# Kernel tuning notes

Hardware: AMD Instinct MI355X
Metric: run time of the kernel (lower is better)

The kernel has to match this reference:

```python
import jax, jax.numpy as jnp
import numpy as np

ALPHA = 0.2  # LeakyReLU negative slope (module init arg)


def setup_inputs() -> dict:
    key = jax.random.key(0)
    ks = jax.random.split(key, 5)
    b, w, K, E = 8, 256, 256, 512  # batch, window_size, n_features, embed (=2*window)
    x = jax.random.normal(ks[0], (b, w, K), dtype=jnp.float32)
    W = jax.random.normal(ks[1], (E, 2 * w), dtype=jnp.float32) * 0.05
    b_lin = jax.random.normal(ks[2], (E,), dtype=jnp.float32) * 0.05
    a = jax.random.normal(ks[3], (E,), dtype=jnp.float32) * 0.05
    bias = jax.random.normal(ks[4], (K, K), dtype=jnp.float32) * 0.05
    return {"x": x, "W": W, "b_lin": b_lin, "a": a, "bias": bias}


def reference(x, W, b_lin, a, bias):
    # x: (b, window, K) -> v: (b, K, window)
    v = jnp.transpose(x, (0, 2, 1))
    w = v.shape[2]
    # lin(concat(v_i, v_j)) == v_i @ Wl^T + v_j @ Wr^T + b_lin  (split weight)
    Wl, Wr = W[:, :w], W[:, w:]
    left = jnp.einsum('bkw,ew->bke', v, Wl)    # (b, K, E)
    right = jnp.einsum('bkw,ew->bke', v, Wr)   # (b, K, E)
    pre = left[:, :, None, :] + right[:, None, :, :] + b_lin  # (b, K, K, E)
    act = jax.nn.leaky_relu(pre, negative_slope=ALPHA)
    e = jnp.einsum('bije,e->bij', act, a) + bias               # (b, K, K)
    attn = jax.nn.softmax(e, axis=2)  # dropout p=0 in eval -> identity
    h = jax.nn.sigmoid(jnp.einsum('bij,bjw->biw', attn, v))    # (b, K, window)
    return jnp.transpose(h, (0, 2, 1))                          # (b, window, K)
```

## Files before the change

kernel.cpp:

```cpp
#include <hip/hip_runtime.h>
#include <math.h>

typedef float f32x4 __attribute__((ext_vector_type(4)));
typedef __bf16 bf16x8 __attribute__((ext_vector_type(8)));
typedef unsigned short u16x8 __attribute__((ext_vector_type(8)));

__device__ __forceinline__ unsigned short f2bf(float f) {
    union { float f; unsigned int u; } v; v.f = f;
    unsigned int u = v.u;
    return (unsigned short)((u + 0x7fffu + ((u >> 16) & 1u)) >> 16);
}
__device__ __forceinline__ float bf_lo(unsigned int d) {
    union { unsigned int u; float f; } v; v.u = d << 16; return v.f;
}
__device__ __forceinline__ float bf_hi(unsigned int d) {
    union { unsigned int u; float f; } v; v.u = d & 0xffff0000u; return v.f;
}
__device__ __forceinline__ unsigned int u4get(const uint4& v, int k) {
    return k == 0 ? v.x : k == 1 ? v.y : k == 2 ? v.z : v.w;
}
__device__ __forceinline__ float sigmoidf_(float v) {
    return 1.f / (1.f + __expf(-v));
}

__global__ __launch_bounds__(256) void mfma_gemm_kernel(
    const float* __restrict__ x,
    const float* __restrict__ W,
    const float* __restrict__ b_lin,
    float* __restrict__ Lp,
    unsigned short* __restrict__ R2)
{
    const int b = blockIdx.y;
    const int t = blockIdx.x;
    const bool left = (t < 32);
    int m0, n0;
    if (left) { m0 = (t >> 3) * 64; n0 = (t & 7) * 64; }
    else      { const int tt = t - 32; m0 = (tt >> 2) * 64; n0 = (tt & 3) * 64; }

    __shared__ unsigned short As[64][72];
    __shared__ unsigned short Bs[64][72];

    unsigned short (*Ts)[72] = left ? As : Bs;
    unsigned short (*Ds)[72] = left ? Bs : As;
    const int cbase = left ? m0 : n0;
    const int rbase = left ? n0 : m0;
    const int coff  = left ? 0 : 256;

    const int tid  = threadIdx.x;
    const int wv   = tid >> 6;
    const int lane = tid & 63;
    const int wy = wv >> 1, wx = wv & 1;
    const int lr = lane & 15;
    const int lk = lane >> 4;

    const float* xb = x + b * 65536;

    f32x4 acc[2][2];
    #pragma unroll
    for (int i = 0; i < 2; i++)
        #pragma unroll
        for (int jj = 0; jj < 2; jj++) acc[i][jj] = (f32x4){0.f, 0.f, 0.f, 0.f};

    const int wl = tid >> 4;
    const int kg = tid & 15;
    const int dr = tid >> 2;
    const int dc = (tid & 3) * 16;

    for (int k0 = 0; k0 < 256; k0 += 64) {
        #pragma unroll
        for (int p = 0; p < 4; p++) {
            const int w = wl + 16 * p;
            const float4 v = *(const float4*)(xb + (k0 + w) * 256 + cbase + kg * 4);
            Ts[kg * 4 + 0][w] = f2bf(v.x);
            Ts[kg * 4 + 1][w] = f2bf(v.y);
            Ts[kg * 4 + 2][w] = f2bf(v.z);
            Ts[kg * 4 + 3][w] = f2bf(v.w);
        }
        {
            const float* src = W + (rbase + dr) * 512 + coff + k0 + dc;
            const float4 v0 = *(const float4*)(src);
            const float4 v1 = *(const float4*)(src + 4);
            const float4 v2 = *(const float4*)(src + 8);
            const float4 v3 = *(const float4*)(src + 12);
            u16x8 o0, o1;
            o0[0] = f2bf(v0.x); o0[1] = f2bf(v0.y); o0[2] = f2bf(v0.z); o0[3] = f2bf(v0.w);
            o0[4] = f2bf(v1.x); o0[5] = f2bf(v1.y); o0[6] = f2bf(v1.z); o0[7] = f2bf(v1.w);
            o1[0] = f2bf(v2.x); o1[1] = f2bf(v2.y); o1[2] = f2bf(v2.z); o1[3] = f2bf(v2.w);
            o1[4] = f2bf(v3.x); o1[5] = f2bf(v3.y); o1[6] = f2bf(v3.z); o1[7] = f2bf(v3.w);
            *(u16x8*)&Ds[dr][dc]     = o0;
            *(u16x8*)&Ds[dr][dc + 8] = o1;
        }
        __syncthreads();
        #pragma unroll
        for (int kk = 0; kk < 64; kk += 32) {
            const bf16x8 a0 = *(const bf16x8*)&As[wy * 32 + lr][kk + lk * 8];
            const bf16x8 a1 = *(const bf16x8*)&As[wy * 32 + 16 + lr][kk + lk * 8];
            const bf16x8 b0 = *(const bf16x8*)&Bs[wx * 32 + lr][kk + lk * 8];
            const bf16x8 b1 = *(const bf16x8*)&Bs[wx * 32 + 16 + lr][kk + lk * 8];
            acc[0][0] = __builtin_amdgcn_mfma_f32_16x16x32_bf16(a0, b0, acc[0][0], 0, 0, 0);
            acc[0][1] = __builtin_amdgcn_mfma_f32_16x16x32_bf16(a0, b1, acc[0][1], 0, 0, 0);
            acc[1][0] = __builtin_amdgcn_mfma_f32_16x16x32_bf16(a1, b0, acc[1][0], 0, 0, 0);
            acc[1][1] = __builtin_amdgcn_mfma_f32_16x16x32_bf16(a1, b1, acc[1][1], 0, 0, 0);
        }
        __syncthreads();
    }

    if (left) {
        #pragma unroll
        for (int mi = 0; mi < 2; mi++) {
            #pragma unroll
            for (int ni = 0; ni < 2; ni++) {
                const int row = m0 + wy * 32 + mi * 16 + lk * 4;
                const int col = n0 + wx * 32 + ni * 16 + lr;
                const float bl = b_lin[col];
                #pragma unroll
                for (int r = 0; r < 4; r++)
                    Lp[b * 131072 + (row + r) * 512 + col] = acc[mi][ni][r] + bl;
            }
        }
    } else {
        unsigned short* R2b = R2 + b * 131072;
        #pragma unroll
        for (int mi = 0; mi < 2; mi++) {
            #pragma unroll
            for (int ni = 0; ni < 2; ni++) {
                const int row = m0 + wy * 32 + mi * 16 + lk * 4;
                const int col = n0 + wx * 32 + ni * 16 + lr;
                ushort4 o;
                o.x = f2bf(acc[mi][ni][0]);
                o.y = f2bf(acc[mi][ni][1]);
                o.z = f2bf(acc[mi][ni][2]);
                o.w = f2bf(acc[mi][ni][3]);
                *(ushort4*)(R2b + (row >> 3) * 2048 + col * 8 + (row & 7)) = o;
            }
        }
    }
}

__global__ __launch_bounds__(512, 3) void attn_kernel(
    const float* __restrict__ x,
    const float* __restrict__ Lp,
    const unsigned int* __restrict__ R2u,
    const float* __restrict__ a,
    const float* __restrict__ bias,
    float* __restrict__ out)
{
    const int b    = blockIdx.x & 7;
    const int i0   = (blockIdx.x >> 3) * 4;
    const int tid  = threadIdx.x;
    const int wv   = tid >> 6;
    const int lane = tid & 63;

    __shared__ float Lt[512][4];
    __shared__ float aS[512];
    __shared__ float acc2P[8][4][256];
    __shared__ float u15s[4];
    __shared__ unsigned short atbf[4 * 264];

    {
        const int i  = tid >> 7;
        const int e0 = (tid & 127) * 4;
        const float4 v = *(const float4*)(Lp + b * 131072 + (i0 + i) * 512 + e0);
        Lt[e0 + 0][i] = v.x;
        Lt[e0 + 1][i] = v.y;
        Lt[e0 + 2][i] = v.z;
        Lt[e0 + 3][i] = v.w;
        aS[tid] = a[tid];
    }

    if (tid < 256) {
        const int i = tid >> 6, ln = tid & 63;
        const float* Lr = Lp + b * 131072 + (i0 + i) * 512 + ln * 8;
        const float* ar = a + ln * 8;
        const float4 la = *(const float4*)Lr;
        const float4 lb = *(const float4*)(Lr + 4);
        const float4 ca = *(const float4*)ar;
        const float4 cb = *(const float4*)(ar + 4);
        float p = la.x * ca.x + la.y * ca.y + la.z * ca.z + la.w * ca.w
                + lb.x * cb.x + lb.y * cb.y + lb.z * cb.z + lb.w * cb.w;
        #pragma unroll
        for (int off = 32; off; off >>= 1) p += __shfl_xor(p, off);
        if (ln == 0) u15s[i] = 0.6f * p;
    }
    __syncthreads();

    const float* aq = aS + wv * 64;
    const float (*Ltq)[4] = (const float (*)[4])(Lt + wv * 64);
    const uint4* Rq = (const uint4*)(R2u + b * 65536) + (wv * 8) * 256 + lane * 4;

    float acc[4][4];
    #pragma unroll
    for (int i = 0; i < 4; i++)
        #pragma unroll
        for (int jj = 0; jj < 4; jj++) acc[i][jj] = 0.f;
    float rsum[4] = {0.f, 0.f, 0.f, 0.f};

    uint4 c0 = Rq[0], c1 = Rq[1], c2 = Rq[2], c3 = Rq[3];
    #pragma unroll 1
    for (int tk = 0; tk < 8; tk++) {
        uint4 n0_, n1_, n2_, n3_;
        if (tk < 7) {
            const uint4* Rn = Rq + (tk + 1) * 256;
            n0_ = Rn[0]; n1_ = Rn[1]; n2_ = Rn[2]; n3_ = Rn[3];
        }
        const float4 av0 = *(const float4*)&aq[tk * 8];
        const float4 av1 = *(const float4*)&aq[tk * 8 + 4];
        #pragma unroll
        for (int s = 0; s < 8; s++) {
            const float4 lv = *(const float4*)Ltq[tk * 8 + s];
            const float ae = (s < 4) ? ((const float*)&av0)[s]
                                     : ((const float*)&av1)[s - 4];
            const int dwi = s >> 1;
            const bool hi = s & 1;
            const float r0 = hi ? bf_hi(u4get(c0, dwi)) : bf_lo(u4get(c0, dwi));
            const float r1 = hi ? bf_hi(u4get(c1, dwi)) : bf_lo(u4get(c1, dwi));
            const float r2 = hi ? bf_hi(u4get(c2, dwi)) : bf_lo(u4get(c2, dwi));
            const float r3 = hi ? bf_hi(u4get(c3, dwi)) : bf_lo(u4get(c3, dwi));
            rsum[0] = fmaf(ae, r0, rsum[0]);
            rsum[1] = fmaf(ae, r1, rsum[1]);
            rsum[2] = fmaf(ae, r2, rsum[2]);
            rsum[3] = fmaf(ae, r3, rsum[3]);
            acc[0][0] = fmaf(ae, fabsf(lv.x + r0), acc[0][0]);
            acc[1][0] = fmaf(ae, fabsf(lv.y + r0), acc[1][0]);
            acc[2][0] = fmaf(ae, fabsf(lv.z + r0), acc[2][0]);
            acc[3][0] = fmaf(ae, fabsf(lv.w + r0), acc[3][0]);
            acc[0][1] = fmaf(ae, fabsf(lv.x + r1), acc[0][1]);
            acc[1][1] = fmaf(ae, fabsf(lv.y + r1), acc[1][1]);
            acc[2][1] = fmaf(ae, fabsf(lv.z + r1), acc[2][1]);
            acc[3][1] = fmaf(ae, fabsf(lv.w + r1), acc[3][1]);
            acc[0][2] = fmaf(ae, fabsf(lv.x + r2), acc[0][2]);
            acc[1][2] = fmaf(ae, fabsf(lv.y + r2), acc[1][2]);
            acc[2][2] = fmaf(ae, fabsf(lv.z + r2), acc[2][2]);
            acc[3][2] = fmaf(ae, fabsf(lv.w + r2), acc[3][2]);
            acc[0][3] = fmaf(ae, fabsf(lv.x + r3), acc[0][3]);
            acc[1][3] = fmaf(ae, fabsf(lv.y + r3), acc[1][3]);
            acc[2][3] = fmaf(ae, fabsf(lv.z + r3), acc[2][3]);
            acc[3][3] = fmaf(ae, fabsf(lv.w + r3), acc[3][3]);
        }
        c0 = n0_; c1 = n1_; c2 = n2_; c3 = n3_;
    }
    #pragma unroll
    for (int i = 0; i < 4; i++)
        #pragma unroll
        for (int jj = 0; jj < 4; jj++)
            acc2P[wv][i][lane * 4 + jj] = fmaf(1.5f, rsum[jj], acc[i][jj]);
    __syncthreads();

    if (tid < 256) {
        const int i = tid >> 6, ln = tid & 63;
        const float u15 = u15s[i];
        float v[4];
        float m = -1e30f;
        #pragma unroll
        for (int u = 0; u < 4; u++) {
            const int jj = ln + 64 * u;
            float ab = 0.f;
            #pragma unroll
            for (int eo = 0; eo < 8; eo++) ab += acc2P[eo][i][jj];
            v[u] = u15 + 0.4f * ab + bias[(i0 + i) * 256 + jj];
            m = fmaxf(m, v[u]);
        }
        #pragma unroll
        for (int off = 32; off; off >>= 1) m = fmaxf(m, __shfl_xor(m, off));
        float s = 0.f;
        #pragma unroll
        for (int u = 0; u < 4; u++) { v[u] = __expf(v[u] - m); s += v[u]; }
        #pragma unroll
        for (int off = 32; off; off >>= 1) s += __shfl_xor(s, off);
        const float inv = 1.f / s;
        #pragma unroll
        for (int u = 0; u < 4; u++)
            atbf[i * 264 + ln + 64 * u] = f2bf(v[u] * inv);
    }
    __syncthreads();

    {
        const int lr = lane & 15;
        const int lk = lane >> 4;
        const int arow = lr & 3;
        #pragma unroll
        for (int half = 0; half < 2; half++) {
            const int nt = wv + half * 8;
            f32x4 hacc = (f32x4){0.f, 0.f, 0.f, 0.f};
            const float* xw = x + b * 65536 + (nt * 16 + lr) * 256;
            #pragma unroll
            for (int kt = 0; kt < 8; kt++) {
                const bf16x8 av = *(const bf16x8*)&atbf[arow * 264 + kt * 32 + lk * 8];
                const float4 f0 = *(const float4*)(xw + kt * 32 + lk * 8);
                const float4 f1 = *(const float4*)(xw + kt * 32 + lk * 8 + 4);
                u16x8 bu;
                bu[0] = f2bf(f0.x); bu[1] = f2bf(f0.y); bu[2] = f2bf(f0.z); bu[3] = f2bf(f0.w);
                bu[4] = f2bf(f1.x); bu[5] = f2bf(f1.y); bu[6] = f2bf(f1.z); bu[7] = f2bf(f1.w);
                const bf16x8 bv = *(const bf16x8*)&bu;
                hacc = __builtin_amdgcn_mfma_f32_16x16x32_bf16(av, bv, hacc, 0, 0, 0);
            }
            if (lk == 0) {
                float4 o;
                o.x = sigmoidf_(hacc[0]);
                o.y = sigmoidf_(hacc[1]);
                o.z = sigmoidf_(hacc[2]);
                o.w = sigmoidf_(hacc[3]);
                *(float4*)(out + b * 65536 + (nt * 16 + lr) * 256 + i0) = o;
            }
        }
    }
}

extern "C" void kernel_launch(void* const* d_in, const int* in_sizes, int n_in,
                              void* d_out, int out_size, void* d_ws, size_t ws_size,
                              hipStream_t stream) {
    const float* x     = (const float*)d_in[0];
    const float* W     = (const float*)d_in[1];
    const float* b_lin = (const float*)d_in[2];
    const float* a     = (const float*)d_in[3];
    const float* bias  = (const float*)d_in[4];
    float* out = (float*)d_out;

    char* ws = (char*)d_ws;
    float*          Lp = (float*)ws;
    unsigned short* R2 = (unsigned short*)(ws + (4 << 20));

    mfma_gemm_kernel<<<dim3(64, 8), 256, 0, stream>>>(x, W, b_lin, Lp, R2);
    attn_kernel<<<512, 512, 0, stream>>>(x, Lp, (const unsigned int*)R2, a, bias, out);
}
```

Measured before the change: 108.9 us.

## Split attention kernel into E-split score kernel and separate softmax epilogue kernel

Divides the embedding reduction across two blocks per (batch, 4-row) tile, doubling the grid of the score kernel and raising its occupancy hint. The partial score sums go to a workspace buffer, and a new epilogue kernel adds the halves, then runs the softmax and the attention-times-x MFMA stage. This exposes more parallelism for the dominant score loop. The cost is an extra kernel launch and a global round trip for the partial scores.

```diff
diff --git a/kernel.cpp b/kernel.cpp
--- a/kernel.cpp
+++ b/kernel.cpp
@@ -137,56 +137,39 @@
     }
 }
 
-__global__ __launch_bounds__(512, 3) void attn_kernel(
-    const float* __restrict__ x,
+__global__ __launch_bounds__(512, 4) void attn_score_kernel(
     const float* __restrict__ Lp,
     const unsigned int* __restrict__ R2u,
     const float* __restrict__ a,
-    const float* __restrict__ bias,
-    float* __restrict__ out)
+    float* __restrict__ P)
 {
     const int b    = blockIdx.x & 7;
-    const int i0   = (blockIdx.x >> 3) * 4;
+    const int ih   = blockIdx.x >> 3;
+    const int i0   = (ih >> 1) * 4;
+    const int half = ih & 1;
     const int tid  = threadIdx.x;
     const int wv   = tid >> 6;
     const int lane = tid & 63;
 
-    __shared__ float Lt[512][4];
-    __shared__ float aS[512];
+    __shared__ float Lt[256][4];
+    __shared__ float aS[256];
     __shared__ float acc2P[8][4][256];
-    __shared__ float u15s[4];
-    __shared__ unsigned short atbf[4 * 264];
 
     {
         const int i  = tid >> 7;
-        const int e0 = (tid & 127) * 4;
-        const float4 v = *(const float4*)(Lp + b * 131072 + (i0 + i) * 512 + e0);
+        const int e0 = (tid & 127) * 2;
+        const float2 v = *(const float2*)(Lp + b * 131072 + (i0 + i) * 512
+                                          + half * 256 + e0);
         Lt[e0 + 0][i] = v.x;
         Lt[e0 + 1][i] = v.y;
-        Lt[e0 + 2][i] = v.z;
-        Lt[e0 + 3][i] = v.w;
-        aS[tid] = a[tid];
-    }
-
-    if (tid < 256) {
-        const int i = tid >> 6, ln = tid & 63;
-        const float* Lr = Lp + b * 131072 + (i0 + i) * 512 + ln * 8;
-        const float* ar = a + ln * 8;
-        const float4 la = *(const float4*)Lr;
-        const float4 lb = *(const float4*)(Lr + 4);
-        const float4 ca = *(const float4*)ar;
-        const float4 cb = *(const float4*)(ar + 4);
-        float p = la.x * ca.x + la.y * ca.y + la.z * ca.z + la.w * ca.w
-                + lb.x * cb.x + lb.y * cb.y + lb.z * cb.z + lb.w * cb.w;
-        #pragma unroll
-        for (int off = 32; off; off >>= 1) p += __shfl_xor(p, off);
-        if (ln == 0) u15s[i] = 0.6f * p;
-    }
+    }
+    if (tid < 256) aS[tid] = a[half * 256 + tid];
     __syncthreads();
 
-    const float* aq = aS + wv * 64;
-    const float (*Ltq)[4] = (const float (*)[4])(Lt + wv * 64);
-    const uint4* Rq = (const uint4*)(R2u + b * 65536) + (wv * 8) * 256 + lane * 4;
+    const float* aq = aS + wv * 32;
+    const float (*Ltq)[4] = (const float (*)[4])(Lt + wv * 32);
+    const uint4* Rq = (const uint4*)(R2u + b * 65536)
+                    + (half * 32 + wv * 4) * 256 + lane * 4;
 
     float acc[4][4];
     #pragma unroll
@@ -197,9 +180,9 @@
 
     uint4 c0 = Rq[0], c1 = Rq[1], c2 = Rq[2], c3 = Rq[3];
     #pragma unroll 1
-    for (int tk = 0; tk < 8; tk++) {
+    for (int tk = 0; tk < 4; tk++) {
         uint4 n0_, n1_, n2_, n3_;
-        if (tk < 7) {
+        if (tk < 3) {
             const uint4* Rn = Rq + (tk + 1) * 256;
             n0_ = Rn[0]; n1_ = Rn[1]; n2_ = Rn[2]; n3_ = Rn[3];
         }
@@ -247,17 +230,62 @@
     __syncthreads();
 
     if (tid < 256) {
-        const int i = tid >> 6, ln = tid & 63;
+        float* Pb = P + blockIdx.x * 1024;
+        #pragma unroll
+        for (int i = 0; i < 4; i++) {
+            float s = 0.f;
+            #pragma unroll
+            for (int eo = 0; eo < 8; eo++) s += acc2P[eo][i][tid];
+            Pb[i * 256 + tid] = s;
+        }
+    }
+}
+
+__global__ __launch_bounds__(512, 2) void attn_epi_kernel(
+    const float* __restrict__ x,
+    const float* __restrict__ Lp,
+    const float* __restrict__ P,
+    const float* __restrict__ a,
+    const float* __restrict__ bias,
+    float* __restrict__ out)
+{
+    const int b    = blockIdx.x & 7;
+    const int i4   = blockIdx.x >> 3;
+    const int i0   = i4 * 4;
+    const int tid  = threadIdx.x;
+    const int wv   = tid >> 6;
+    const int lane = tid & 63;
+
+    __shared__ float u15s[4];
+    __shared__ unsigned short atbf[4 * 264];
+
+    if (tid < 256) {
+        const int i = wv;
+        const float* Lr = Lp + b * 131072 + (i0 + i) * 512 + lane * 8;
+        const float* ar = a + lane * 8;
+        const float4 la = *(const float4*)Lr;
+        const float4 lb = *(const float4*)(Lr + 4);
+        const float4 ca = *(const float4*)ar;
+        const float4 cb = *(const float4*)(ar + 4);
+        float p = la.x * ca.x + la.y * ca.y + la.z * ca.z + la.w * ca.w
+                + lb.x * cb.x + lb.y * cb.y + lb.z * cb.z + lb.w * cb.w;
+        #pragma unroll
+        for (int off = 32; off; off >>= 1) p += __shfl_xor(p, off);
+        if (lane == 0) u15s[i] = 0.6f * p;
+    }
+    __syncthreads();
+
+    if (tid < 256) {
+        const int i = wv;
         const float u15 = u15s[i];
+        const float* P0 = P + ((i4 * 2 + 0) * 8 + b) * 1024 + i * 256;
+        const float* P1 = P + ((i4 * 2 + 1) * 8 + b) * 1024 + i * 256;
         float v[4];
         float m = -1e30f;
         #pragma unroll
         for (int u = 0; u < 4; u++) {
-            const int jj = ln + 64 * u;
-            float ab = 0.f;
-            #pragma unroll
-            for (int eo = 0; eo < 8; eo++) ab += acc2P[eo][i][jj];
-            v[u] = u15 + 0.4f * ab + bias[(i0 + i) * 256 + jj];
+            const int jj = lane + 64 * u;
+            v[u] = u15 + 0.4f * (P0[jj] + P1[jj]) + bias[(i0 + i) * 256 + jj];
             m = fmaxf(m, v[u]);
         }
         #pragma unroll
@@ -270,7 +298,7 @@
         const float inv = 1.f / s;
         #pragma unroll
         for (int u = 0; u < 4; u++)
-            atbf[i * 264 + ln + 64 * u] = f2bf(v[u] * inv);
+            atbf[i * 264 + lane + 64 * u] = f2bf(v[u] * inv);
     }
     __syncthreads();
 
@@ -319,7 +347,9 @@
     char* ws = (char*)d_ws;
     float*          Lp = (float*)ws;
     unsigned short* R2 = (unsigned short*)(ws + (4 << 20));
+    float*          P  = (float*)(ws + (6 << 20));
 
     mfma_gemm_kernel<<<dim3(64, 8), 256, 0, stream>>>(x, W, b_lin, Lp, R2);
-    attn_kernel<<<512, 512, 0, stream>>>(x, Lp, (const unsigned int*)R2, a, bias, out);
-}
+    attn_score_kernel<<<1024, 512, 0, stream>>>(Lp, (const unsigned int*)R2, a, P);
+    attn_epi_kernel<<<512, 512, 0, stream>>>(x, Lp, P, a, bias, out);
+}
```

Measured after the change: 111.1 us. 1.02x slower.
